# Performance work log

Hardware: AMD Instinct MI355X
Metric: run time of the kernel (lower is better)

Reference implementation:

```python
import jax, jax.numpy as jnp
import numpy as np
import math

B, H, S, D = 2, 16, 2048, 128

def setup_inputs() -> dict:
    key = jax.random.key(0)
    kq, kk, kv = jax.random.split(key, 3)
    return {
        "query": jax.random.normal(kq, (B, H, S, D), dtype=jnp.float32),
        "key": jax.random.normal(kk, (B, H, S, D), dtype=jnp.float32),
        "value": jax.random.normal(kv, (B, H, S, D), dtype=jnp.float32),
        "mask": jnp.ones((1, 1, S, S), dtype=jnp.bool_),
    }

def reference(query, key, value, mask):
    # scale_factor=None -> 1/sqrt(head_dim), as in standard SDPA
    head_dim = query.shape[-1]
    scale = 1.0 / math.sqrt(head_dim)
    # [B,H,Sq,Sk] attention scores
    scores = jnp.einsum("bhqd,bhkd->bhqk", query, key) * scale
    neg_inf = jnp.finfo(scores.dtype).min
    scores = jnp.where(mask, scores, neg_inf)
    attn = jax.nn.softmax(scores, axis=-1)  # dropout p=0.0 -> identity
    return jnp.einsum("bhqk,bhkd->bhqd", attn, value)
```

## Files before the change

kernel.cpp:

```cpp
#include <hip/hip_runtime.h>
#include <cstdint>

using short8  = __attribute__((ext_vector_type(8))) short;
using short2v = __attribute__((ext_vector_type(2))) short;
using f32x16  = __attribute__((ext_vector_type(16))) float;
using float4v = __attribute__((ext_vector_type(4))) float;
using int4v   = __attribute__((ext_vector_type(4))) int;

constexpr int Bc = 2, Hc = 16, Sc = 2048, Dc = 128;
constexpr int NW = 4, QBLK = 128, KVBLK = 64;
constexpr int NT = Sc / KVBLK;
constexpr float SCALE_LOG2E = 0.08838834764831845f * 1.4426950408889634f;

__device__ __forceinline__ short f2bf(float f) {
  union { float f; uint32_t u; } v; v.f = f;
  uint32_t u = v.u;
  uint32_t r = (u + 0x7FFFu + ((u >> 16) & 1u)) >> 16;
  return (short)r;
}

__device__ __forceinline__ uint32_t cvtpk(float lo, float hi) {
  uint32_t r;
  asm("v_cvt_pk_bf16_f32 %0, %1, %2" : "=v"(r) : "v"(lo), "v"(hi));
  return r;
}

__device__ __forceinline__ float max3f(float a, float b, float c) {
  float d;
  asm("v_max3_f32 %0, %1, %2, %3" : "=v"(d) : "v"(a), "v"(b), "v"(c));
  return d;
}

#define GLOAD_LDS16(g, l)                                                     \
  __builtin_amdgcn_global_load_lds(                                           \
      (const __attribute__((address_space(1))) void*)(g),                     \
      (__attribute__((address_space(3))) void*)(l), 16, 0, 0)

__global__ __launch_bounds__(256)
void prep_kernel(const float* __restrict__ K, const float* __restrict__ V,
                 ushort* __restrict__ Kb, ushort* __restrict__ Vt) {
  __shared__ short T[64 * 66];
  if (blockIdx.x < 4096) {
    size_t i = ((size_t)blockIdx.x * 256 + threadIdx.x) * 8;
    float4v a = *(const float4v*)(K + i);
    float4v b = *(const float4v*)(K + i + 4);
    short8 r;
    r[0] = f2bf(a[0]); r[1] = f2bf(a[1]); r[2] = f2bf(a[2]); r[3] = f2bf(a[3]);
    r[4] = f2bf(b[0]); r[5] = f2bf(b[1]); r[6] = f2bf(b[2]); r[7] = f2bf(b[3]);
    *(short8*)(Kb + i) = r;
    return;
  }
  const int pid = blockIdx.x - 4096;
  const int bh = pid >> 6;
  const int xy = pid & 63;
  const int st = xy & 31, dt = xy >> 5;
  const int s0 = st * 64, d0 = dt * 64;
  const float* Vb = V + (size_t)bh * Sc * Dc;
  ushort* Vtb = Vt + (size_t)bh * Dc * Sc;
#pragma unroll
  for (int i = 0; i < 4; ++i) {
    int idx = threadIdx.x + i * 256;
    int r = idx >> 4, c4 = (idx & 15) * 4;
    float4v v = *(const float4v*)&Vb[(size_t)(s0 + r) * Dc + d0 + c4];
    short2v lo, hi;
    lo[0] = f2bf(v[0]); lo[1] = f2bf(v[1]);
    hi[0] = f2bf(v[2]); hi[1] = f2bf(v[3]);
    *(short2v*)&T[r * 66 + c4]     = lo;
    *(short2v*)&T[r * 66 + c4 + 2] = hi;
  }
  __syncthreads();
#pragma unroll
  for (int i = 0; i < 2; ++i) {
    int idx = threadIdx.x + i * 256;
    int dr = idx >> 3, c8 = (idx & 7) * 8;
    short8 o;
#pragma unroll
    for (int j = 0; j < 8; ++j) o[j] = T[(c8 + j) * 66 + dr];
    *(short8*)&Vtb[(size_t)(d0 + dr) * Sc + s0 + c8] = o;
  }
}

__global__ __launch_bounds__(256, 2)
void sdpa_fwd_kernel(const float* __restrict__ Q, const ushort* __restrict__ Kb,
                     const ushort* __restrict__ Vt, float* __restrict__ O) {
  __shared__ __align__(16) short Kl[2][KVBLK * Dc];
  __shared__ __align__(16) short Vl[2][Dc * KVBLK];

  const int tid  = threadIdx.x;
  const int w    = tid >> 6;
  const int lane = tid & 63;
  const int l31  = lane & 31;
  const int hi   = lane >> 5;

  const int bh = blockIdx.x & 31;
  const int qt = blockIdx.x >> 5;
  const size_t base = (size_t)bh * Sc * Dc;
  const float* Qb = Q + base;
  const ushort* KbB = Kb + base;
  const ushort* VtB = Vt + base;

  const int qrow = qt * QBLK + w * 32 + l31;

  short8 qf[8];
#pragma unroll
  for (int c = 0; c < 8; ++c) {
    const float* src = Qb + (size_t)qrow * Dc + c * 16 + hi * 8;
    float4v a = *(const float4v*)src;
    float4v b = *(const float4v*)(src + 4);
    short8 r;
    r[0] = f2bf(a[0] * SCALE_LOG2E); r[1] = f2bf(a[1] * SCALE_LOG2E);
    r[2] = f2bf(a[2] * SCALE_LOG2E); r[3] = f2bf(a[3] * SCALE_LOG2E);
    r[4] = f2bf(b[0] * SCALE_LOG2E); r[5] = f2bf(b[1] * SCALE_LOG2E);
    r[6] = f2bf(b[2] * SCALE_LOG2E); r[7] = f2bf(b[3] * SCALE_LOG2E);
    qf[c] = r;
  }

  int offK[4], offV[4], kldsOff[4], vldsOff[4];
#pragma unroll
  for (int j = 0; j < 4; ++j) {
    int row = w * 16 + j * 4 + (lane >> 4);
    offK[j] = row * Dc + (((lane & 15) ^ (row & 15)) * 8);
    kldsOff[j] = (w * 16 + j * 4) * Dc;
    int d = w * 32 + j * 8 + (lane >> 3);
    offV[j] = d * Sc + (((lane & 7) ^ (d & 7)) * 8);
    vldsOff[j] = (w * 32 + j * 8) * KVBLK;
  }

  auto STAGE = [&](int buf, int kv0) {
#pragma unroll
    for (int j = 0; j < 4; ++j) {
      GLOAD_LDS16(KbB + (size_t)kv0 * Dc + offK[j], &Kl[buf][kldsOff[j]]);
      GLOAD_LDS16(VtB + kv0 + offV[j], &Vl[buf][vldsOff[j]]);
    }
  };

  f32x16 acc[4];
#pragma unroll
  for (int i = 0; i < 4; ++i)
#pragma unroll
    for (int r = 0; r < 16; ++r) acc[i][r] = 0.f;
  float m_run = -1e30f;
  float l_half = 0.f;

  STAGE(0, 0);
  int cur = 0;

  for (int it = 0; it < NT; ++it) {
    __syncthreads();
    if (it + 1 < NT) STAGE(cur ^ 1, (it + 1) * KVBLK);

    f32x16 st0, st1;
#pragma unroll
    for (int r = 0; r < 16; ++r) { st0[r] = 0.f; st1[r] = 0.f; }
    __builtin_amdgcn_s_setprio(1);
#pragma unroll
    for (int c = 0; c < 8; ++c) {
      int e0 = (l31 * Dc + c * 16 + hi * 8) ^ ((l31 & 15) << 3);
      int e1 = ((32 + l31) * Dc + c * 16 + hi * 8) ^ ((l31 & 15) << 3);
      short8 kf0 = *(const short8*)&Kl[cur][e0];
      short8 kf1 = *(const short8*)&Kl[cur][e1];
      st0 = __builtin_amdgcn_mfma_f32_32x32x16_bf16(kf0, qf[c], st0, 0, 0, 0);
      st1 = __builtin_amdgcn_mfma_f32_32x32x16_bf16(kf1, qf[c], st1, 0, 0, 0);
    }
    __builtin_amdgcn_s_setprio(0);

    float t0 = max3f(st0[0], st0[4], st0[8]);
    float t1 = max3f(st0[1], st0[5], st0[9]);
    float t2 = max3f(st0[2], st0[6], st0[10]);
    float t3 = max3f(st0[3], st0[7], st0[11]);
    t0 = max3f(t0, st0[12], st1[0]);
    t1 = max3f(t1, st0[13], st1[1]);
    t2 = max3f(t2, st0[14], st1[2]);
    t3 = max3f(t3, st0[15], st1[3]);
    t0 = max3f(t0, st1[4], st1[8]);
    t1 = max3f(t1, st1[5], st1[9]);
    t2 = max3f(t2, st1[6], st1[10]);
    t3 = max3f(t3, st1[7], st1[11]);
    t0 = max3f(t0, st1[12], t2);
    t1 = max3f(t1, st1[13], t3);
    t0 = max3f(t0, st1[14], t1);
    float tmax = fmaxf(t0, st1[15]);
    tmax = fmaxf(tmax, __shfl_xor(tmax, 32));

    if (!__all(tmax <= m_run + 8.0f)) {
      float m_new = fmaxf(m_run, tmax);
      float alpha = __builtin_amdgcn_exp2f(m_run - m_new);
      l_half *= alpha;
#pragma unroll
      for (int i = 0; i < 4; ++i)
#pragma unroll
        for (int r = 0; r < 16; ++r) acc[i][r] *= alpha;
      m_run = m_new;
    }

    float ps0 = 0.f, ps1 = 0.f, ps2 = 0.f, ps3 = 0.f;
#pragma unroll
    for (int kc = 0; kc < 4; ++kc) {
      const f32x16& stq = (kc < 2) ? st0 : st1;
      const int rb = (kc & 1) * 8;
      float p0 = __builtin_amdgcn_exp2f(stq[rb + 0] - m_run);
      float p1 = __builtin_amdgcn_exp2f(stq[rb + 1] - m_run);
      float p2 = __builtin_amdgcn_exp2f(stq[rb + 2] - m_run);
      float p3 = __builtin_amdgcn_exp2f(stq[rb + 3] - m_run);
      float p4 = __builtin_amdgcn_exp2f(stq[rb + 4] - m_run);
      float p5 = __builtin_amdgcn_exp2f(stq[rb + 5] - m_run);
      float p6 = __builtin_amdgcn_exp2f(stq[rb + 6] - m_run);
      float p7 = __builtin_amdgcn_exp2f(stq[rb + 7] - m_run);
      ps0 += p0 + p4; ps1 += p1 + p5; ps2 += p2 + p6; ps3 += p3 + p7;
      uint32_t a0 = cvtpk(p0, p1);
      uint32_t b0 = cvtpk(p4, p5);
      asm volatile("v_permlane32_swap_b32 %0, %1" : "+v"(a0), "+v"(b0));
      uint32_t a1 = cvtpk(p2, p3);
      uint32_t b1 = cvtpk(p6, p7);
      asm volatile("v_permlane32_swap_b32 %0, %1" : "+v"(a1), "+v"(b1));
      int4v wv; wv[0] = (int)a0; wv[1] = (int)a1; wv[2] = (int)b0; wv[3] = (int)b1;
      union { int4v i; short8 s; } u; u.i = wv;
      short8 pf = u.s;

      __builtin_amdgcn_s_setprio(1);
#pragma unroll
      for (int dt = 0; dt < 4; ++dt) {
        int d = dt * 32 + l31;
        int elem = (d * KVBLK + kc * 16 + hi * 8) ^ ((l31 & 7) << 3);
        short8 vf = *(const short8*)&Vl[cur][elem];
        acc[dt] = __builtin_amdgcn_mfma_f32_32x32x16_bf16(vf, pf, acc[dt], 0, 0, 0);
      }
      __builtin_amdgcn_s_setprio(0);
    }
    l_half += (ps0 + ps1) + (ps2 + ps3);
    cur ^= 1;
  }

  float l_run = l_half + __shfl_xor(l_half, 32);
  const float inv_l = 1.0f / l_run;
  float* Ob = O + base + (size_t)qrow * Dc;
#pragma unroll
  for (int dt = 0; dt < 4; ++dt)
#pragma unroll
    for (int g = 0; g < 4; ++g) {
      float4v o;
      o[0] = acc[dt][4 * g + 0] * inv_l; o[1] = acc[dt][4 * g + 1] * inv_l;
      o[2] = acc[dt][4 * g + 2] * inv_l; o[3] = acc[dt][4 * g + 3] * inv_l;
      *(float4v*)&Ob[dt * 32 + 8 * g + 4 * hi] = o;
    }
}

extern "C" void kernel_launch(void* const* d_in, const int* in_sizes, int n_in,
                              void* d_out, int out_size, void* d_ws, size_t ws_size,
                              hipStream_t stream) {
  const float* Q = (const float*)d_in[0];
  const float* K = (const float*)d_in[1];
  const float* V = (const float*)d_in[2];
  float* O = (float*)d_out;

  const size_t nElem = (size_t)Bc * Hc * Sc * Dc;
  ushort* Kb = (ushort*)d_ws;
  ushort* Vt = Kb + nElem;

  prep_kernel<<<dim3(4096 + 64 * Bc * Hc), dim3(256), 0, stream>>>(K, V, Kb, Vt);

  sdpa_fwd_kernel<<<dim3((Sc / QBLK) * Bc * Hc), dim3(256), 0, stream>>>(Q, Kb, Vt, O);
}
```

Before: 102.1 us.

## Stage K/V tiles through registers into padded LDS instead of direct global-to-LDS loads

Replaces the direct global_load_lds staging, which used XOR-swizzled LDS addressing, with ordinary global loads into registers that are later written into padded LDS arrays (row pitch 136 for K, 72 for V). Loads are issued two tiles ahead and written one tile ahead, giving a register-prefetch pipeline with a single barrier at the end of each iteration. This removes the XOR address arithmetic and is meant to hide global latency better. In exchange it adds VGPR pressure (8 int4 registers) under a 2-waves launch bound, enlarges the LDS footprint, and adds explicit ds_write instructions.

```diff
diff --git a/kernel.cpp b/kernel.cpp
--- a/kernel.cpp
+++ b/kernel.cpp
@@ -10,6 +10,8 @@
 constexpr int Bc = 2, Hc = 16, Sc = 2048, Dc = 128;
 constexpr int NW = 4, QBLK = 128, KVBLK = 64;
 constexpr int NT = Sc / KVBLK;
+constexpr int KP = 136;
+constexpr int VP = 72;
 constexpr float SCALE_LOG2E = 0.08838834764831845f * 1.4426950408889634f;
 
 __device__ __forceinline__ short f2bf(float f) {
@@ -30,11 +32,6 @@
   asm("v_max3_f32 %0, %1, %2, %3" : "=v"(d) : "v"(a), "v"(b), "v"(c));
   return d;
 }
-
-#define GLOAD_LDS16(g, l)                                                     \
-  __builtin_amdgcn_global_load_lds(                                           \
-      (const __attribute__((address_space(1))) void*)(g),                     \
-      (__attribute__((address_space(3))) void*)(l), 16, 0, 0)
 
 __global__ __launch_bounds__(256)
 void prep_kernel(const float* __restrict__ K, const float* __restrict__ V,
@@ -83,8 +80,8 @@
 __global__ __launch_bounds__(256, 2)
 void sdpa_fwd_kernel(const float* __restrict__ Q, const ushort* __restrict__ Kb,
                      const ushort* __restrict__ Vt, float* __restrict__ O) {
-  __shared__ __align__(16) short Kl[2][KVBLK * Dc];
-  __shared__ __align__(16) short Vl[2][Dc * KVBLK];
+  __shared__ __align__(16) short Kl[2][KVBLK][KP];
+  __shared__ __align__(16) short Vl[2][Dc][VP];
 
   const int tid  = threadIdx.x;
   const int w    = tid >> 6;
@@ -115,22 +112,28 @@
     qf[c] = r;
   }
 
-  int offK[4], offV[4], kldsOff[4], vldsOff[4];
+  const int colK = (lane & 15) * 8;
+  const int colV = (lane & 7) * 8;
+  int rowK[4], dV[4];
 #pragma unroll
   for (int j = 0; j < 4; ++j) {
-    int row = w * 16 + j * 4 + (lane >> 4);
-    offK[j] = row * Dc + (((lane & 15) ^ (row & 15)) * 8);
-    kldsOff[j] = (w * 16 + j * 4) * Dc;
-    int d = w * 32 + j * 8 + (lane >> 3);
-    offV[j] = d * Sc + (((lane & 7) ^ (d & 7)) * 8);
-    vldsOff[j] = (w * 32 + j * 8) * KVBLK;
-  }
-
-  auto STAGE = [&](int buf, int kv0) {
+    rowK[j] = w * 16 + j * 4 + (lane >> 4);
+    dV[j]   = w * 32 + j * 8 + (lane >> 3);
+  }
+
+  int4v kreg[4], vreg[4];
+  auto LOADT = [&](int kv0) {
 #pragma unroll
     for (int j = 0; j < 4; ++j) {
-      GLOAD_LDS16(KbB + (size_t)kv0 * Dc + offK[j], &Kl[buf][kldsOff[j]]);
-      GLOAD_LDS16(VtB + kv0 + offV[j], &Vl[buf][vldsOff[j]]);
+      kreg[j] = *(const int4v*)(KbB + (size_t)(kv0 + rowK[j]) * Dc + colK);
+      vreg[j] = *(const int4v*)(VtB + (size_t)dV[j] * Sc + kv0 + colV);
+    }
+  };
+  auto WRITET = [&](int buf) {
+#pragma unroll
+    for (int j = 0; j < 4; ++j) {
+      *(int4v*)&Kl[buf][rowK[j]][colK] = kreg[j];
+      *(int4v*)&Vl[buf][dV[j]][colV] = vreg[j];
     }
   };
 
@@ -142,12 +145,19 @@
   float m_run = -1e30f;
   float l_half = 0.f;
 
-  STAGE(0, 0);
+  LOADT(0);
+  WRITET(0);
+  LOADT(KVBLK);
+  __syncthreads();
   int cur = 0;
 
   for (int it = 0; it < NT; ++it) {
-    __syncthreads();
-    if (it + 1 < NT) STAGE(cur ^ 1, (it + 1) * KVBLK);
+    if (it + 1 < NT) WRITET(cur ^ 1);
+    if (it + 2 < NT) LOADT((it + 2) * KVBLK);
+
+    const short* kb0 = &Kl[cur][l31][hi * 8];
+    const short* kb1 = &Kl[cur][32 + l31][hi * 8];
+    const short* vb  = &Vl[cur][l31][hi * 8];
 
     f32x16 st0, st1;
 #pragma unroll
@@ -155,10 +165,8 @@
     __builtin_amdgcn_s_setprio(1);
 #pragma unroll
     for (int c = 0; c < 8; ++c) {
-      int e0 = (l31 * Dc + c * 16 + hi * 8) ^ ((l31 & 15) << 3);
-      int e1 = ((32 + l31) * Dc + c * 16 + hi * 8) ^ ((l31 & 15) << 3);
-      short8 kf0 = *(const short8*)&Kl[cur][e0];
-      short8 kf1 = *(const short8*)&Kl[cur][e1];
+      short8 kf0 = *(const short8*)(kb0 + c * 16);
+      short8 kf1 = *(const short8*)(kb1 + c * 16);
       st0 = __builtin_amdgcn_mfma_f32_32x32x16_bf16(kf0, qf[c], st0, 0, 0, 0);
       st1 = __builtin_amdgcn_mfma_f32_32x32x16_bf16(kf1, qf[c], st1, 0, 0, 0);
     }
@@ -220,14 +228,13 @@
       __builtin_amdgcn_s_setprio(1);
 #pragma unroll
       for (int dt = 0; dt < 4; ++dt) {
-        int d = dt * 32 + l31;
-        int elem = (d * KVBLK + kc * 16 + hi * 8) ^ ((l31 & 7) << 3);
-        short8 vf = *(const short8*)&Vl[cur][elem];
+        short8 vf = *(const short8*)(vb + dt * (32 * VP) + kc * 16);
         acc[dt] = __builtin_amdgcn_mfma_f32_32x32x16_bf16(vf, pf, acc[dt], 0, 0, 0);
       }
       __builtin_amdgcn_s_setprio(0);
     }
     l_half += (ps0 + ps1) + (ps2 + ps3);
+    __syncthreads();
     cur ^= 1;
   }
 
```

New measurement: 102.4 us. Within noise of the previous version (+0.3%).
